# Kernel optimization log

Hardware: AMD Instinct MI355X
Metric: run time of the kernel (lower is better)

## Reference

```python
import jax, jax.numpy as jnp
import numpy as np

B, T, C, NH = 4, 2048, 1024, 16
HD = C // NH  # head dim = 64


def setup_inputs() -> dict:
    key = jax.random.key(0)
    ks = jax.random.split(key, 5)
    s = 0.02
    return {
        "x": jax.random.normal(ks[0], (B, T, C), dtype=jnp.float32),
        "W_attn": jax.random.normal(ks[1], (C, 3 * C), dtype=jnp.float32) * s,
        "b_attn": jnp.zeros((3 * C,), dtype=jnp.float32),
        "W_proj": jax.random.normal(ks[2], (C, C), dtype=jnp.float32) * s,
        "b_proj": jnp.zeros((C,), dtype=jnp.float32),
    }


def reference(x, W_attn, b_attn, W_proj, b_proj):
    Bv, Tv, Cv = x.shape
    qkv = x @ W_attn + b_attn  # [B,T,3C]
    q, k, v = jnp.split(qkv, 3, axis=2)
    # [B,T,C] -> [B,NH,T,HD]
    def heads(t):
        return t.reshape(Bv, Tv, NH, HD).transpose(0, 2, 1, 3)
    q, k, v = heads(q), heads(k), heads(v)
    scores = jnp.einsum("bhqd,bhkd->bhqk", q, k) / jnp.sqrt(jnp.float32(HD))
    causal = jnp.tril(jnp.ones((Tv, Tv), dtype=bool))
    scores = jnp.where(causal[None, None, :, :], scores, jnp.float32(-jnp.inf))
    probs = jax.nn.softmax(scores, axis=-1)
    # dropout rate is 0.0 -> identity
    y = jnp.einsum("bhqk,bhkd->bhqd", probs, v)
    y = y.transpose(0, 2, 1, 3).reshape(Bv, Tv, Cv)
    return y @ W_proj + b_proj
```

## Files before the change

### kernel.cpp

```cpp
#include <hip/hip_runtime.h>
#include <hip/hip_bf16.h>

#define Bsz 4
#define Tseq 2048
#define Cdim 1024
#define NH 16
#define HD 64
#define Mrows (Bsz*Tseq)
#define N3C (3*Cdim)

typedef __attribute__((ext_vector_type(8))) short short8;
typedef __attribute__((ext_vector_type(4))) short short4v;
typedef __attribute__((ext_vector_type(4))) float float4v;

__device__ __forceinline__ unsigned short f2b(float f) {
    union { float f; unsigned u; } x; x.f = f;
    unsigned u = x.u;
    u += 0x7fff + ((u >> 16) & 1);
    return (unsigned short)(u >> 16);
}

__device__ __forceinline__ unsigned pk2bf(float a, float b) {
#if __has_builtin(__builtin_amdgcn_cvt_pk_bf16_f32)
    auto w = __builtin_amdgcn_cvt_pk_bf16_f32(a, b);
    unsigned u; __builtin_memcpy(&u, &w, 4);
    return u;
#else
    return (unsigned)f2b(a) | ((unsigned)f2b(b) << 16);
#endif
}

#define GLDS(gp, lp) __builtin_amdgcn_global_load_lds(                         \
    (const __attribute__((address_space(1))) unsigned*)(gp),                   \
    (__attribute__((address_space(3))) unsigned*)(lp), 16, 0, 0)

__global__ __launch_bounds__(256) void cast_kernel(const float* __restrict__ in,
                                                   unsigned short* __restrict__ out, int n) {
    int i = (blockIdx.x * 256 + threadIdx.x) * 4;
    if (i < n) {
        float4 v = *reinterpret_cast<const float4*>(in + i);
        ushort4 o;
        o.x = f2b(v.x); o.y = f2b(v.y); o.z = f2b(v.z); o.w = f2b(v.w);
        *reinterpret_cast<ushort4*>(out + i) = o;
    }
}

__global__ __launch_bounds__(256) void transpose_cast(const float* __restrict__ in,
                                                      unsigned short* __restrict__ out,
                                                      int K, int N) {
    __shared__ float tile[32][33];
    int n0 = blockIdx.x * 32, k0 = blockIdx.y * 32;
    int tx = threadIdx.x & 31, ty = threadIdx.x >> 5;
    #pragma unroll
    for (int i = 0; i < 32; i += 8)
        tile[ty + i][tx] = in[(k0 + ty + i) * N + n0 + tx];
    __syncthreads();
    #pragma unroll
    for (int i = 0; i < 32; i += 8)
        out[(size_t)(n0 + ty + i) * K + k0 + tx] = f2b(tile[tx][ty + i]);
}


template<int MI, int BN, bool QKV>
__global__ __launch_bounds__(512, 2) void gemm2p(const unsigned short* __restrict__ A,
                                                 const unsigned short* __restrict__ Bt,
                                                 const float* __restrict__ bias,
                                                 unsigned short* __restrict__ qb,
                                                 unsigned short* __restrict__ kb,
                                                 unsigned short* __restrict__ vb,
                                                 float* __restrict__ out) {
    __shared__ unsigned short As[2][2][256 * 32];
    __shared__ unsigned short Bs[2][2][BN * 32];

    constexpr int WN = (MI == 8) ? 4 : 2;
    constexpr int SPP = 2 + BN / 128;
    constexpr int NCOLB = (QKV ? N3C : Cdim) / BN;

    int tid = threadIdx.x;
    int lane = tid & 63, wave = tid >> 6;
    int wm = wave / WN, wn = wave % WN;
    int l15 = lane & 15, quad = lane >> 4;
    int wmBase = wm * (MI * 16);

    int f = blockIdx.x;
    int xcd = f & 7, slot = f >> 3;
    int rowblk = xcd * 4 + (slot & 3);
    int colblk = slot >> 2;
    int row0 = rowblk * 256;
    int col0 = colblk * BN;
    (void)NCOLB;

    int srow4 = lane >> 2;
    int gsrc = ((lane & 3) ^ ((lane >> 3) & 3)) * 8;
    const unsigned short* Ag = A + (size_t)(row0 + srow4) * Cdim + gsrc;
    const unsigned short* Bg = Bt + (size_t)(col0 + srow4) * Cdim + gsrc;

    #define STG_AB(sph_, kk_, sb_) do {                                         \
        GLDS(Ag + (size_t)(wave * 16) * Cdim + (kk_),                           \
             &As[sb_][sph_][(wave * 16) * 32]);                                 \
        GLDS(Ag + (size_t)(128 + wave * 16) * Cdim + (kk_),                     \
             &As[sb_][sph_][(128 + wave * 16) * 32]);                           \
        GLDS(Bg + (size_t)(wave * 16) * Cdim + (kk_),                           \
             &Bs[sb_][sph_][(wave * 16) * 32]);                                 \
        if constexpr (BN == 256)                                                \
            GLDS(Bg + (size_t)(128 + wave * 16) * Cdim + (kk_),                 \
                 &Bs[sb_][sph_][(128 + wave * 16) * 32]);                       \
    } while (0)

    float4v acc[MI][4] = {};

    STG_AB(0, 0, 0);
    STG_AB(1, 32, 0);
    STG_AB(0, 64, 1);
    if constexpr (SPP == 4) asm volatile("s_waitcnt vmcnt(8)" ::: "memory");
    else                    asm volatile("s_waitcnt vmcnt(6)" ::: "memory");
    __builtin_amdgcn_s_barrier();

    int gq0 = (quad ^ ((l15 >> 1) & 3)) * 8;
    int afb = (wmBase + l15) * 32 + gq0;
    int bfb = (wn * 64 + l15) * 32 + gq0;

    #pragma unroll 1
    for (int t = 0; t < 16; ++t) {
        #pragma unroll
        for (int ph = 0; ph < 2; ++ph) {
            int bc = t & 1;
            const unsigned short* Asl = &As[bc][ph][0];
            const unsigned short* Bsl = &Bs[bc][ph][0];

            short8 af[MI], bf[4];
            #pragma unroll
            for (int mi = 0; mi < MI; mi++)
                af[mi] = *(const short8*)&Asl[afb + mi * 512];
            #pragma unroll
            for (int nj = 0; nj < 4; nj++)
                bf[nj] = *(const short8*)&Bsl[bfb + nj * 512];

            int s = (2 * t + ph + 3) & 31;
            int st_ = s >> 1, sph = s & 1, sb = st_ & 1;
            STG_AB(sph, st_ * 64 + sph * 32, sb);

            if constexpr (SPP == 4) asm volatile("s_waitcnt vmcnt(8)" ::: "memory");
            else                    asm volatile("s_waitcnt vmcnt(6)" ::: "memory");
            __builtin_amdgcn_s_barrier();
            asm volatile("s_waitcnt lgkmcnt(0)" ::: "memory");
            __builtin_amdgcn_sched_barrier(0);
            __builtin_amdgcn_s_setprio(1);
            #pragma unroll
            for (int mi = 0; mi < MI; mi++)
                #pragma unroll
                for (int nj = 0; nj < 4; nj++)
                    acc[mi][nj] = __builtin_amdgcn_mfma_f32_16x16x32_bf16(af[mi], bf[nj], acc[mi][nj], 0, 0, 0);
            __builtin_amdgcn_s_setprio(0);
            __builtin_amdgcn_s_barrier();
        }
    }
    asm volatile("s_waitcnt vmcnt(0)" ::: "memory");
    #undef STG_AB

    #pragma unroll
    for (int mi = 0; mi < MI; mi++) {
        #pragma unroll
        for (int nj = 0; nj < 4; nj++) {
            int colb = col0 + wn * 64 + nj * 16 + l15;
            int rowb = row0 + wmBase + mi * 16 + quad * 4;
            if (QKV) {
                int p = colb >> 10;
                int h = (colb & 1023) >> 6;
                int d = colb & 63;
                int b = rowb >> 11;
                int t = rowb & 2047;
                if (p == 2) {
                    ushort4 pk;
                    pk.x = f2b(acc[mi][nj][0] + bias[colb]);
                    pk.y = f2b(acc[mi][nj][1] + bias[colb]);
                    pk.z = f2b(acc[mi][nj][2] + bias[colb]);
                    pk.w = f2b(acc[mi][nj][3] + bias[colb]);
                    *(ushort4*)&vb[((size_t)(b * NH + h) * HD + d) * Tseq + t] = pk;
                } else {
                    unsigned short* dst = (p == 0) ? qb : kb;
                    #pragma unroll
                    for (int r = 0; r < 4; r++)
                        dst[((size_t)(b * NH + h) * Tseq + (t + r)) * HD + d] =
                            f2b(acc[mi][nj][r] + bias[colb]);
                }
            } else {
                #pragma unroll
                for (int r = 0; r < 4; r++)
                    out[(size_t)(rowb + r) * Cdim + colb] = acc[mi][nj][r] + bias[colb];
            }
        }
    }
}


__global__ __launch_bounds__(256, 4) void attn_kernel(const unsigned short* __restrict__ qb,
                                                      const unsigned short* __restrict__ kb,
                                                      const unsigned short* __restrict__ vt,
                                                      unsigned short* __restrict__ yb) {
    __shared__ unsigned short Ks[2][64 * 64];
    __shared__ unsigned short Vs[2][64 * 64];

    int tid = threadIdx.x;
    int lane = tid & 63, wave = tid >> 6;
    int l15 = lane & 15, quad = lane >> 4;
    int bh = blockIdx.x;
    int qt = 15 - blockIdx.y;

    const unsigned short* Qh = qb + (size_t)bh * Tseq * HD;
    const unsigned short* Kh = kb + (size_t)bh * Tseq * HD;
    const unsigned short* Vh = vt + (size_t)bh * HD * Tseq;
    int b = bh >> 4, h = bh & 15;
    const float cexp = 0.18033688011112042f;

    int q0 = qt * 128;
    int rb0 = q0 + wave * 32;

    short8 qf[2][2];
    #pragma unroll
    for (int mi = 0; mi < 2; mi++)
        #pragma unroll
        for (int g = 0; g < 2; g++)
            qf[mi][g] = *(const short8*)(Qh + (size_t)(rb0 + mi * 16 + l15) * HD + g * 32 + quad * 8);

    int srow = lane >> 3;
    int scol = ((lane & 7) ^ srow) * 8;
    const unsigned short* Kg0 = Kh + (size_t)(wave * 16 + srow) * HD + scol;
    const unsigned short* Vg0 = Vh + (size_t)(wave * 16 + srow) * Tseq + scol;
    unsigned short* Kl0 = &Ks[0][wave * 1024];
    unsigned short* Vl0 = &Vs[0][wave * 1024];
    unsigned short* Kl1 = &Ks[1][wave * 1024];
    unsigned short* Vl1 = &Vs[1][wave * 1024];

    int sx = l15 & 7;
    int kx0 = (quad ^ sx) * 8;
    int kx1 = ((4 + quad) ^ sx) * 8;
    int qh_ = quad >> 1, ql_ = quad & 1;

    float4v ov[2][4] = {};
    float m[2]  = {-1e30f, -1e30f};
    float lp[2] = {0.f, 0.f};

    int nw = (q0 >> 6) + 2;

    GLDS(Kg0, Kl0);                GLDS(Kg0 + 8 * HD, Kl0 + 512);
    GLDS(Vg0, Vl0);                GLDS(Vg0 + 8 * Tseq, Vl0 + 512);
    __syncthreads();

    #pragma unroll 1
    for (int it = 0; it < nw; ++it) {
        int j0 = it << 6;

        if (it + 1 < nw) {
            int jn = j0 + 64;
            unsigned short* Kl = (it & 1) ? Kl0 : Kl1;
            unsigned short* Vl = (it & 1) ? Vl0 : Vl1;
            GLDS(Kg0 + (size_t)jn * HD, Kl);
            GLDS(Kg0 + (size_t)(jn + 8) * HD, Kl + 512);
            GLDS(Vg0 + jn, Vl);
            GLDS(Vg0 + 8 * Tseq + jn, Vl + 512);
        }

        if (j0 <= rb0 + 31) {
            const unsigned short* Kl = &Ks[it & 1][0];
            const unsigned short* Vl = &Vs[it & 1][0];

            float4v st[2][4];
            #pragma unroll
            for (int mi = 0; mi < 2; mi++)
                #pragma unroll
                for (int kg = 0; kg < 4; kg++)
                    st[mi][kg] = (float4v){0.f, 0.f, 0.f, 0.f};
            #pragma unroll
            for (int kg = 0; kg < 4; kg++) {
                int krow = kg * 1024 + l15 * 64;
                short8 kf0 = *(const short8*)&Kl[krow + kx0];
                short8 kf1 = *(const short8*)&Kl[krow + kx1];
                st[0][kg] = __builtin_amdgcn_mfma_f32_16x16x32_bf16(kf0, qf[0][0], st[0][kg], 0, 0, 0);
                st[0][kg] = __builtin_amdgcn_mfma_f32_16x16x32_bf16(kf1, qf[0][1], st[0][kg], 0, 0, 0);
                st[1][kg] = __builtin_amdgcn_mfma_f32_16x16x32_bf16(kf0, qf[1][0], st[1][kg], 0, 0, 0);
                st[1][kg] = __builtin_amdgcn_mfma_f32_16x16x32_bf16(kf1, qf[1][1], st[1][kg], 0, 0, 0);
            }

            if (j0 + 63 > rb0) {
                #pragma unroll
                for (int mi = 0; mi < 2; mi++) {
                    int qrow = rb0 + mi * 16 + l15;
                    #pragma unroll
                    for (int kg = 0; kg < 4; kg++) {
                        int keyb = j0 + kg * 16 + quad * 4;
                        #pragma unroll
                        for (int r = 0; r < 4; r++)
                            if (keyb + r > qrow) st[mi][kg][r] = -1e30f;
                    }
                }
            }

            short4v pf[2][4];
            #pragma unroll
            for (int mi = 0; mi < 2; mi++) {
                float mx = st[mi][0][0];
                #pragma unroll
                for (int kg = 0; kg < 4; kg++)
                    #pragma unroll
                    for (int r = 0; r < 4; r++)
                        mx = fmaxf(mx, st[mi][kg][r]);
                mx = fmaxf(mx, __shfl_xor(mx, 16));
                mx = fmaxf(mx, __shfl_xor(mx, 32));
                if (__any(mx > m[mi] + 16.0f)) {
                    float mn = fmaxf(m[mi], mx);
                    float alv = __builtin_amdgcn_exp2f((m[mi] - mn) * cexp);
                    m[mi] = mn;
                    lp[mi] *= alv;
                    float ar_[4];
                    #pragma unroll
                    for (int r = 0; r < 4; r++)
                        ar_[r] = __shfl(alv, quad * 4 + r);
                    #pragma unroll
                    for (int dg = 0; dg < 4; dg++)
                        #pragma unroll
                        for (int r = 0; r < 4; r++)
                            ov[mi][dg][r] *= ar_[r];
                }
                float mc = -m[mi] * cexp;
                float sum = 0.f;
                #pragma unroll
                for (int kg = 0; kg < 4; kg++) {
                    float p0 = __builtin_amdgcn_exp2f(__builtin_fmaf(st[mi][kg][0], cexp, mc));
                    float p1 = __builtin_amdgcn_exp2f(__builtin_fmaf(st[mi][kg][1], cexp, mc));
                    float p2 = __builtin_amdgcn_exp2f(__builtin_fmaf(st[mi][kg][2], cexp, mc));
                    float p3 = __builtin_amdgcn_exp2f(__builtin_fmaf(st[mi][kg][3], cexp, mc));
                    sum += (p0 + p1) + (p2 + p3);
                    union { unsigned u[2]; short4v s; } pk_;
                    pk_.u[0] = pk2bf(p0, p1);
                    pk_.u[1] = pk2bf(p2, p3);
                    pf[mi][kg] = pk_.s;
                }
                lp[mi] += sum;
            }

            #pragma unroll
            for (int kg = 0; kg < 4; kg++) {
                int vx = (((kg * 2 + qh_) ^ sx) << 3) + ql_ * 4;
                #pragma unroll
                for (int dg = 0; dg < 4; dg++) {
                    short4v vf = *(const short4v*)&Vl[dg * 1024 + l15 * 64 + vx];
                    ov[0][dg] = __builtin_amdgcn_mfma_f32_16x16x16bf16_1k(pf[0][kg], vf, ov[0][dg], 0, 0, 0);
                    ov[1][dg] = __builtin_amdgcn_mfma_f32_16x16x16bf16_1k(pf[1][kg], vf, ov[1][dg], 0, 0, 0);
                }
            }
        }

        __syncthreads();
    }

    #pragma unroll
    for (int mi = 0; mi < 2; mi++) {
        float lf = lp[mi];
        lf += __shfl_xor(lf, 16);
        lf += __shfl_xor(lf, 32);
        float rinv[4];
        #pragma unroll
        for (int r = 0; r < 4; r++)
            rinv[r] = 1.0f / __shfl(lf, quad * 4 + r);
        #pragma unroll
        for (int dg = 0; dg < 4; dg++)
            #pragma unroll
            for (int r = 0; r < 4; r++) {
                int t = rb0 + mi * 16 + quad * 4 + r;
                yb[((size_t)b * Tseq + t) * Cdim + h * HD + dg * 16 + l15] =
                    f2b(ov[mi][dg][r] * rinv[r]);
            }
    }
}

extern "C" void kernel_launch(void* const* d_in, const int* in_sizes, int n_in,
                              void* d_out, int out_size, void* d_ws, size_t ws_size,
                              hipStream_t stream) {
    const float* x  = (const float*)d_in[0];
    const float* Wa = (const float*)d_in[1];
    const float* ba = (const float*)d_in[2];
    const float* Wp = (const float*)d_in[3];
    const float* bp = (const float*)d_in[4];
    float* out = (float*)d_out;

    unsigned short* ws = (unsigned short*)d_ws;
    unsigned short* xb  = ws;
    unsigned short* Wat = xb  + (size_t)Mrows * Cdim;
    unsigned short* Wpt = Wat + (size_t)N3C * Cdim;
    unsigned short* qb  = Wpt + (size_t)Cdim * Cdim;
    unsigned short* kb  = qb  + (size_t)Bsz * NH * Tseq * HD;
    unsigned short* vb  = kb  + (size_t)Bsz * NH * Tseq * HD;
    unsigned short* yb  = vb  + (size_t)Bsz * NH * Tseq * HD;

    int nx = Mrows * Cdim;
    cast_kernel<<<nx / 4 / 256, 256, 0, stream>>>(x, xb, nx);
    transpose_cast<<<dim3(N3C / 32, Cdim / 32), 256, 0, stream>>>(Wa, Wat, Cdim, N3C);
    transpose_cast<<<dim3(Cdim / 32, Cdim / 32), 256, 0, stream>>>(Wp, Wpt, Cdim, Cdim);

    gemm2p<8, 256, true><<<384, 512, 0, stream>>>(xb, Wat, ba, qb, kb, vb, nullptr);

    attn_kernel<<<dim3(Bsz * NH, 16), 256, 0, stream>>>(qb, kb, vb, yb);

    gemm2p<4, 128, false><<<256, 512, 0, stream>>>(yb, Wpt, bp, nullptr, nullptr, nullptr, out);
}
```

Baseline: 253.9 us.

## Replace double-buffered two-phase GEMM with three-stage single-barrier pipeline

Both GEMMs now use one kernel with a 256x128 tile, a three-slot LDS ring of 32-wide K slices, and one barrier per K step instead of two barriers per phase. The QKV GEMM moves from 256x256 tiles on 384 blocks to 256x128 tiles on 768 blocks, with launch bounds raised to 4 blocks per CU. The smaller LDS footprint and fewer barriers are meant to raise occupancy and cut synchronisation stalls. In exchange each tile reuses less data per load, and the deeper prefetch relies on the vmcnt counts matching the three loads issued per stage.

```diff
diff --git a/kernel.cpp b/kernel.cpp
--- a/kernel.cpp
+++ b/kernel.cpp
@@ -61,109 +61,127 @@
 }
 
 
-template<int MI, int BN, bool QKV>
-__global__ __launch_bounds__(512, 2) void gemm2p(const unsigned short* __restrict__ A,
+template<bool QKV>
+__global__ __launch_bounds__(512, 4) void gemm3s(const unsigned short* __restrict__ A,
                                                  const unsigned short* __restrict__ Bt,
                                                  const float* __restrict__ bias,
                                                  unsigned short* __restrict__ qb,
                                                  unsigned short* __restrict__ kb,
                                                  unsigned short* __restrict__ vb,
                                                  float* __restrict__ out) {
-    __shared__ unsigned short As[2][2][256 * 32];
-    __shared__ unsigned short Bs[2][2][BN * 32];
-
-    constexpr int WN = (MI == 8) ? 4 : 2;
-    constexpr int SPP = 2 + BN / 128;
-    constexpr int NCOLB = (QKV ? N3C : Cdim) / BN;
+    __shared__ unsigned short As[3][256 * 32];
+    __shared__ unsigned short Bs[3][128 * 32];
 
     int tid = threadIdx.x;
     int lane = tid & 63, wave = tid >> 6;
-    int wm = wave / WN, wn = wave % WN;
+    int wm = wave >> 1, wn = wave & 1;
     int l15 = lane & 15, quad = lane >> 4;
-    int wmBase = wm * (MI * 16);
 
     int f = blockIdx.x;
     int xcd = f & 7, slot = f >> 3;
     int rowblk = xcd * 4 + (slot & 3);
     int colblk = slot >> 2;
     int row0 = rowblk * 256;
-    int col0 = colblk * BN;
-    (void)NCOLB;
+    int col0 = colblk * 128;
 
     int srow4 = lane >> 2;
     int gsrc = ((lane & 3) ^ ((lane >> 3) & 3)) * 8;
     const unsigned short* Ag = A + (size_t)(row0 + srow4) * Cdim + gsrc;
     const unsigned short* Bg = Bt + (size_t)(col0 + srow4) * Cdim + gsrc;
 
-    #define STG_AB(sph_, kk_, sb_) do {                                         \
-        GLDS(Ag + (size_t)(wave * 16) * Cdim + (kk_),                           \
-             &As[sb_][sph_][(wave * 16) * 32]);                                 \
-        GLDS(Ag + (size_t)(128 + wave * 16) * Cdim + (kk_),                     \
-             &As[sb_][sph_][(128 + wave * 16) * 32]);                           \
-        GLDS(Bg + (size_t)(wave * 16) * Cdim + (kk_),                           \
-             &Bs[sb_][sph_][(wave * 16) * 32]);                                 \
-        if constexpr (BN == 256)                                                \
-            GLDS(Bg + (size_t)(128 + wave * 16) * Cdim + (kk_),                 \
-                 &Bs[sb_][sph_][(128 + wave * 16) * 32]);                       \
+    #define STG3(kk_, sl_) do {                                                \
+        GLDS(Ag + (size_t)(wave * 16) * Cdim + (kk_),                          \
+             &As[sl_][(wave * 16) * 32]);                                      \
+        GLDS(Ag + (size_t)(128 + wave * 16) * Cdim + (kk_),                    \
+             &As[sl_][(128 + wave * 16) * 32]);                                \
+        GLDS(Bg + (size_t)(wave * 16) * Cdim + (kk_),                          \
+             &Bs[sl_][(wave * 16) * 32]);                                      \
     } while (0)
 
-    float4v acc[MI][4] = {};
-
-    STG_AB(0, 0, 0);
-    STG_AB(1, 32, 0);
-    STG_AB(0, 64, 1);
-    if constexpr (SPP == 4) asm volatile("s_waitcnt vmcnt(8)" ::: "memory");
-    else                    asm volatile("s_waitcnt vmcnt(6)" ::: "memory");
+    float4v acc[4][4] = {};
+
+    STG3(0, 0);
+    STG3(32, 1);
+    asm volatile("s_waitcnt vmcnt(3)" ::: "memory");
     __builtin_amdgcn_s_barrier();
 
     int gq0 = (quad ^ ((l15 >> 1) & 3)) * 8;
-    int afb = (wmBase + l15) * 32 + gq0;
+    int afb = (wm * 64 + l15) * 32 + gq0;
     int bfb = (wn * 64 + l15) * 32 + gq0;
 
+    int sl = 0, sp = 2;
     #pragma unroll 1
-    for (int t = 0; t < 16; ++t) {
-        #pragma unroll
-        for (int ph = 0; ph < 2; ++ph) {
-            int bc = t & 1;
-            const unsigned short* Asl = &As[bc][ph][0];
-            const unsigned short* Bsl = &Bs[bc][ph][0];
-
-            short8 af[MI], bf[4];
-            #pragma unroll
-            for (int mi = 0; mi < MI; mi++)
-                af[mi] = *(const short8*)&Asl[afb + mi * 512];
+    for (int p = 0; p < 30; ++p) {
+        const unsigned short* Asl = &As[sl][0];
+        const unsigned short* Bsl = &Bs[sl][0];
+        short8 af[4], bf[4];
+        #pragma unroll
+        for (int mi = 0; mi < 4; mi++)
+            af[mi] = *(const short8*)&Asl[afb + mi * 512];
+        #pragma unroll
+        for (int nj = 0; nj < 4; nj++)
+            bf[nj] = *(const short8*)&Bsl[bfb + nj * 512];
+
+        STG3((p + 2) * 32, sp);
+
+        __builtin_amdgcn_s_setprio(1);
+        #pragma unroll
+        for (int mi = 0; mi < 4; mi++)
             #pragma unroll
             for (int nj = 0; nj < 4; nj++)
-                bf[nj] = *(const short8*)&Bsl[bfb + nj * 512];
-
-            int s = (2 * t + ph + 3) & 31;
-            int st_ = s >> 1, sph = s & 1, sb = st_ & 1;
-            STG_AB(sph, st_ * 64 + sph * 32, sb);
-
-            if constexpr (SPP == 4) asm volatile("s_waitcnt vmcnt(8)" ::: "memory");
-            else                    asm volatile("s_waitcnt vmcnt(6)" ::: "memory");
-            __builtin_amdgcn_s_barrier();
-            asm volatile("s_waitcnt lgkmcnt(0)" ::: "memory");
-            __builtin_amdgcn_sched_barrier(0);
-            __builtin_amdgcn_s_setprio(1);
-            #pragma unroll
-            for (int mi = 0; mi < MI; mi++)
-                #pragma unroll
-                for (int nj = 0; nj < 4; nj++)
-                    acc[mi][nj] = __builtin_amdgcn_mfma_f32_16x16x32_bf16(af[mi], bf[nj], acc[mi][nj], 0, 0, 0);
-            __builtin_amdgcn_s_setprio(0);
-            __builtin_amdgcn_s_barrier();
-        }
-    }
-    asm volatile("s_waitcnt vmcnt(0)" ::: "memory");
-    #undef STG_AB
+                acc[mi][nj] = __builtin_amdgcn_mfma_f32_16x16x32_bf16(af[mi], bf[nj], acc[mi][nj], 0, 0, 0);
+        __builtin_amdgcn_s_setprio(0);
+
+        asm volatile("s_waitcnt vmcnt(3)" ::: "memory");
+        __builtin_amdgcn_s_barrier();
+        sl = (sl == 2) ? 0 : sl + 1;
+        sp = (sp == 2) ? 0 : sp + 1;
+    }
+    {
+        const unsigned short* Asl = &As[sl][0];
+        const unsigned short* Bsl = &Bs[sl][0];
+        short8 af[4], bf[4];
+        #pragma unroll
+        for (int mi = 0; mi < 4; mi++)
+            af[mi] = *(const short8*)&Asl[afb + mi * 512];
+        #pragma unroll
+        for (int nj = 0; nj < 4; nj++)
+            bf[nj] = *(const short8*)&Bsl[bfb + nj * 512];
+        __builtin_amdgcn_s_setprio(1);
+        #pragma unroll
+        for (int mi = 0; mi < 4; mi++)
+            #pragma unroll
+            for (int nj = 0; nj < 4; nj++)
+                acc[mi][nj] = __builtin_amdgcn_mfma_f32_16x16x32_bf16(af[mi], bf[nj], acc[mi][nj], 0, 0, 0);
+        __builtin_amdgcn_s_setprio(0);
+        asm volatile("s_waitcnt vmcnt(0)" ::: "memory");
+        __builtin_amdgcn_s_barrier();
+        sl = (sl == 2) ? 0 : sl + 1;
+    }
+    {
+        const unsigned short* Asl = &As[sl][0];
+        const unsigned short* Bsl = &Bs[sl][0];
+        short8 af[4], bf[4];
+        #pragma unroll
+        for (int mi = 0; mi < 4; mi++)
+            af[mi] = *(const short8*)&Asl[afb + mi * 512];
+        #pragma unroll
+        for (int nj = 0; nj < 4; nj++)
+            bf[nj] = *(const short8*)&Bsl[bfb + nj * 512];
+        #pragma unroll
+        for (int mi = 0; mi < 4; mi++)
+            #pragma unroll
+            for (int nj = 0; nj < 4; nj++)
+                acc[mi][nj] = __builtin_amdgcn_mfma_f32_16x16x32_bf16(af[mi], bf[nj], acc[mi][nj], 0, 0, 0);
+    }
+    #undef STG3
 
     #pragma unroll
-    for (int mi = 0; mi < MI; mi++) {
+    for (int mi = 0; mi < 4; mi++) {
         #pragma unroll
         for (int nj = 0; nj < 4; nj++) {
             int colb = col0 + wn * 64 + nj * 16 + l15;
-            int rowb = row0 + wmBase + mi * 16 + quad * 4;
+            int rowb = row0 + wm * 64 + mi * 16 + quad * 4;
             if (QKV) {
                 int p = colb >> 10;
                 int h = (colb & 1023) >> 6;
@@ -398,9 +416,9 @@
     transpose_cast<<<dim3(N3C / 32, Cdim / 32), 256, 0, stream>>>(Wa, Wat, Cdim, N3C);
     transpose_cast<<<dim3(Cdim / 32, Cdim / 32), 256, 0, stream>>>(Wp, Wpt, Cdim, Cdim);
 
-    gemm2p<8, 256, true><<<384, 512, 0, stream>>>(xb, Wat, ba, qb, kb, vb, nullptr);
+    gemm3s<true><<<768, 512, 0, stream>>>(xb, Wat, ba, qb, kb, vb, nullptr);
 
     attn_kernel<<<dim3(Bsz * NH, 16), 256, 0, stream>>>(qb, kb, vb, yb);
 
-    gemm2p<4, 128, false><<<256, 512, 0, stream>>>(yb, Wpt, bp, nullptr, nullptr, nullptr, out);
-}
+    gemm3s<false><<<256, 512, 0, stream>>>(yb, Wpt, bp, nullptr, nullptr, nullptr, out);
+}
```

New measurement: 242.6 us. 4.5% less time.
